# Kernel tuning notes

Measured on AMD Instinct MI355X. Metric: run time of the kernel, lower is better.

Reference implementation:

```python
import jax, jax.numpy as jnp
import numpy as np

N, E, G = 30000, 120000, 256
F_IN, F_E, H, T = 16, 8, 32, 10
EPS = 1e-5


def setup_inputs() -> dict:
    key = jax.random.key(0)
    ks = jax.random.split(key, 16)
    s = 0.05
    inp = {
        'x': jax.random.normal(ks[0], (N, F_IN), jnp.float32),
        'edge_attr': jax.random.normal(ks[1], (E, F_E), jnp.float32),
        'edge_index': jax.random.randint(ks[2], (2, E), 0, N),
        'batch': jnp.sort(jax.random.randint(ks[3], (N,), 0, G)),
        'c1_nn_w': jax.random.normal(ks[4], (F_E, F_IN * H), jnp.float32) * s,
        'c1_nn_b': jnp.zeros((F_IN * H,), jnp.float32),
        'c1_root': jax.random.normal(ks[5], (F_IN, H), jnp.float32) * s,
        'c1_bias': jnp.zeros((H,), jnp.float32),
        'c2_nn_w': jax.random.normal(ks[6], (F_E, H * H), jnp.float32) * s,
        'c2_nn_b': jnp.zeros((H * H,), jnp.float32),
        'c2_root': jax.random.normal(ks[7], (H, H), jnp.float32) * s,
        'c2_bias': jnp.zeros((H,), jnp.float32),
        'c3_nn_w': jax.random.normal(ks[8], (F_E, H * H), jnp.float32) * s,
        'c3_nn_b': jnp.zeros((H * H,), jnp.float32),
        'c3_root': jax.random.normal(ks[9], (H, H), jnp.float32) * s,
        'c3_bias': jnp.zeros((H,), jnp.float32),
        'bn1_g': jnp.ones((H,), jnp.float32), 'bn1_b': jnp.zeros((H,), jnp.float32),
        'bn1_m': jnp.zeros((H,), jnp.float32), 'bn1_v': jnp.ones((H,), jnp.float32),
        'bn2_g': jnp.ones((H,), jnp.float32), 'bn2_b': jnp.zeros((H,), jnp.float32),
        'bn2_m': jnp.zeros((H,), jnp.float32), 'bn2_v': jnp.ones((H,), jnp.float32),
        'mlp_w1': jax.random.normal(ks[10], (H, H), jnp.float32) * s,
        'mlp_b1': jnp.zeros((H,), jnp.float32),
        'mlp_w2': jax.random.normal(ks[11], (H, T), jnp.float32) * s,
        'mlp_b2': jnp.zeros((T,), jnp.float32),
    }
    return inp


def _nnconv(x, edge_index, edge_attr, nn_w, nn_b, root, bias, in_dim, out_dim):
    # per-edge weight matrix from edge features: [E, in_dim, out_dim]
    W = (edge_attr @ nn_w + nn_b).reshape(-1, in_dim, out_dim)
    # gather source node features, per-edge matvec, scatter-add to targets
    msg = jnp.einsum('ei,eio->eo', x[edge_index[0]], W)
    agg = jax.ops.segment_sum(msg, edge_index[1], num_segments=N)
    return agg + x @ root + bias


def _graph_size_norm(x, batch):
    deg = jax.ops.segment_sum(jnp.ones((N,), x.dtype), batch, num_segments=G)
    inv_sqrt = jnp.where(deg > 0, deg, 1.0) ** -0.5
    return x * inv_sqrt[batch][:, None]


def _bn_eval(x, g, b, m, v):
    return (x - m) * (g * jax.lax.rsqrt(v + EPS)) + b


def reference(x, edge_attr, edge_index, batch,
              c1_nn_w, c1_nn_b, c1_root, c1_bias,
              c2_nn_w, c2_nn_b, c2_root, c2_bias,
              c3_nn_w, c3_nn_b, c3_root, c3_bias,
              bn1_g, bn1_b, bn1_m, bn1_v,
              bn2_g, bn2_b, bn2_m, bn2_v,
              mlp_w1, mlp_b1, mlp_w2, mlp_b2):
    h = _nnconv(x, edge_index, edge_attr, c1_nn_w, c1_nn_b, c1_root, c1_bias, F_IN, H)
    h = _graph_size_norm(h, batch)
    h = jax.nn.relu(_bn_eval(h, bn1_g, bn1_b, bn1_m, bn1_v))
    h = _nnconv(h, edge_index, edge_attr, c2_nn_w, c2_nn_b, c2_root, c2_bias, H, H)
    h = _graph_size_norm(h, batch)
    h = jax.nn.relu(_bn_eval(h, bn2_g, bn2_b, bn2_m, bn2_v))
    h = _nnconv(h, edge_index, edge_attr, c3_nn_w, c3_nn_b, c3_root, c3_bias, H, H)
    # global mean pool over graphs
    cnt = jax.ops.segment_sum(jnp.ones((N,), h.dtype), batch, num_segments=G)
    pooled = jax.ops.segment_sum(h, batch, num_segments=G) / jnp.maximum(cnt, 1.0)[:, None]
    # MLP head (dropout inactive in eval)
    out = jax.nn.relu(pooled @ mlp_w1 + mlp_b1) @ mlp_w2 + mlp_b2
    return out
```

## Files before the change

kernel.cpp:

```cpp
#include <hip/hip_runtime.h>

#define NN 30000
#define NE 120000
#define NG 256
#define FIN 16
#define HD 32
#define TOUT 10
#define EPSV 1e-5f
#define NB_SCAN 30

__device__ __forceinline__ void atomAddF(float* p, float v) {
    unsafeAtomicAdd(p, v);
}

__global__ __launch_bounds__(256) void count_deg_kernel(
    const int* __restrict__ eidx, const int* __restrict__ batch,
    int* __restrict__ deg_in, float* __restrict__ deg_g)
{
    const int t = blockIdx.x * 256 + threadIdx.x;
    if (t < NE) atomicAdd(&deg_in[eidx[NE + t]], 1);

    const int lane = threadIdx.x & 63;
    const int g = (t < NN) ? batch[t] : -1;
    const int prev = __shfl_up(g, 1);
    const bool head = (lane == 0) || (g != prev);
    const unsigned long long heads = __ballot(head);
    if (head && g >= 0) {
        const unsigned long long higher =
            (lane < 63) ? (heads >> (lane + 1)) : 0ULL;
        const int next = higher ? (lane + __ffsll(higher)) : 64;
        atomAddF(&deg_g[g], (float)(next - lane));
    }
}

__global__ __launch_bounds__(1024) void scan_phase1(
    const int* __restrict__ deg_in, int* __restrict__ row_start,
    int* __restrict__ blocksum)
{
    __shared__ int wsum[16];
    const int t = threadIdx.x, lane = t & 63, w = t >> 6;
    const int idx = blockIdx.x * 1024 + t;
    const int v = (idx < NN) ? deg_in[idx] : 0;
    int s = v;
    #pragma unroll
    for (int off = 1; off < 64; off <<= 1) {
        const int u = __shfl_up(s, off, 64);
        if (lane >= off) s += u;
    }
    if (lane == 63) wsum[w] = s;
    __syncthreads();
    if (w == 0) {
        int ws = (lane < 16) ? wsum[lane] : 0;
        #pragma unroll
        for (int off = 1; off < 16; off <<= 1) {
            const int u = __shfl_up(ws, off, 64);
            if (lane >= off) ws += u;
        }
        if (lane < 16) wsum[lane] = ws;
    }
    __syncthreads();
    const int incl = s + ((w > 0) ? wsum[w - 1] : 0);
    if (idx < NN) row_start[idx] = incl - v;
    if (t == 1023) blocksum[blockIdx.x] = incl;
}

__global__ __launch_bounds__(1024) void scan_apply(
    const int* __restrict__ blocksum, int* __restrict__ row_start,
    int* __restrict__ cursor)
{
    __shared__ int boff_s;
    const int t = threadIdx.x;
    if (t < 64) {
        int v = (t < blockIdx.x) ? blocksum[t] : 0;
        #pragma unroll
        for (int off = 32; off > 0; off >>= 1) v += __shfl_down(v, off, 64);
        if (t == 0) boff_s = v;
    }
    __syncthreads();
    const int idx = blockIdx.x * 1024 + t;
    if (idx < NN) {
        const int r = row_start[idx] + boff_s;
        row_start[idx] = r;
        cursor[idx]    = r;
    }
    if (blockIdx.x == 0 && t == 0) row_start[NN] = NE;
}

__global__ __launch_bounds__(256) void csr_scatter(
    const int* __restrict__ eidx, const float* __restrict__ ea,
    int* __restrict__ cursor,
    int* __restrict__ src_s,
    float4* __restrict__ ea_s)
{
    const int e = blockIdx.x * 256 + threadIdx.x;
    if (e < NE) {
        const int d = eidx[NE + e];
        const int slot = atomicAdd(&cursor[d], 1);
        src_s[slot] = eidx[e];
        const float4* s4 = (const float4*)(ea + (size_t)e * 8);
        ea_s[2 * slot]     = s4[0];
        ea_s[2 * slot + 1] = s4[1];
    }
    if (e < 8) src_s[NE + e] = 0;
}

template<int IN, bool FINAL>
__global__ __launch_bounds__(256) void fused_layer(
    const float* __restrict__ hin,
    const int*   __restrict__ src_s,
    const float4* __restrict__ ea_s,
    const int*   __restrict__ row_start,
    const float* __restrict__ nn_w,
    const float* __restrict__ nn_b,
    const float* __restrict__ root,
    const float* __restrict__ bias,
    const int*   __restrict__ batch,
    const float* __restrict__ deg_g,
    const float* __restrict__ bn_g,
    const float* __restrict__ bn_b,
    const float* __restrict__ bn_m,
    const float* __restrict__ bn_v,
    float*       __restrict__ out)
{
    constexpr int K  = 10 * IN;
    constexpr int KQ = K / 4;
    constexpr int KL = KQ / 2;
    constexpr int NQ = 32 / IN;

    __shared__ float Tlds[16 * K];
    __shared__ float P[4 * 16 * 64];

    const int tid = threadIdx.x;
    const int wv  = tid >> 6;
    const int l   = tid & 63;
    const int h   = l >> 5;
    const int o   = l & 31;
    const int l5  = l & 31;
    const int pr  = l >> 5;

    float Wreg[KL];
    const int kbase = wv * KQ + h * KL;
    #pragma unroll
    for (int kk = 0; kk < KL; ++kk) {
        const int k = kbase + kk;
        const float* src = (k < 8 * IN) ? (nn_w + k * 32)
                         : (k < 9 * IN) ? (nn_b + (k - 8 * IN) * 32)
                                        : (root + (k - 9 * IN) * 32);
        Wreg[kk] = src[o];
    }

    const int i = l5 & (IN - 1);
    const int q = l5 / IN;

    #pragma unroll
    for (int j = 0; j < 2; ++j) {
        const int nloc = wv * 4 + j * 2 + pr;
        const int d    = blockIdx.x * 16 + nloc;

        float t[9];
        #pragma unroll
        for (int f = 0; f < 9; ++f) t[f] = 0.0f;

        const int p0 = row_start[d];
        const int p1 = row_start[d + 1];

        int p = p0 + q;
        if (p < p1) {
            int pn     = p + NQ;
            int s_cur  = src_s[p];
            int s_nxt  = src_s[pn];
            float4 a_c = ea_s[2 * p];
            float4 b_c = ea_s[2 * p + 1];
            float  xv  = hin[(long)s_cur * IN + i];

            while (true) {
                const float4 a_n = ea_s[2 * pn];
                const float4 b_n = ea_s[2 * pn + 1];
                const float  xvn = hin[(long)s_nxt * IN + i];
                const int pn2    = pn + NQ;
                const int s_n2   = src_s[pn2];

                t[0] = fmaf(a_c.x, xv, t[0]);
                t[1] = fmaf(a_c.y, xv, t[1]);
                t[2] = fmaf(a_c.z, xv, t[2]);
                t[3] = fmaf(a_c.w, xv, t[3]);
                t[4] = fmaf(b_c.x, xv, t[4]);
                t[5] = fmaf(b_c.y, xv, t[5]);
                t[6] = fmaf(b_c.z, xv, t[6]);
                t[7] = fmaf(b_c.w, xv, t[7]);
                t[8] += xv;

                p = pn;
                if (p >= p1) break;
                pn = pn2; s_nxt = s_n2;
                a_c = a_n; b_c = b_n; xv = xvn;
            }
        }

        if (IN == 16) {
            #pragma unroll
            for (int f = 0; f < 9; ++f) t[f] += __shfl_xor(t[f], 16, 64);
        }

        if (l5 < IN) {
            float* tb = Tlds + nloc * K;
            #pragma unroll
            for (int f = 0; f < 9; ++f) tb[f * IN + i] = t[f];
            tb[9 * IN + i] = hin[(long)d * IN + i];
        }
    }
    __syncthreads();

    for (int n = 0; n < 16; ++n) {
        const float* tb = Tlds + n * K + kbase;
        float acc = 0.0f;
        #pragma unroll
        for (int kq = 0; kq < KL / 4; ++kq) {
            const float4 tv = *(const float4*)(tb + kq * 4);
            acc = fmaf(Wreg[4 * kq + 0], tv.x, acc);
            acc = fmaf(Wreg[4 * kq + 1], tv.y, acc);
            acc = fmaf(Wreg[4 * kq + 2], tv.z, acc);
            acc = fmaf(Wreg[4 * kq + 3], tv.w, acc);
        }
        P[(wv * 16 + n) * 64 + l] = acc;
    }
    __syncthreads();

    #pragma unroll
    for (int r = 0; r < 2; ++r) {
        const int idx = r * 256 + tid;
        const int n   = idx >> 5;
        const int oo  = idx & 31;
        float sum = bias[oo];
        #pragma unroll
        for (int ww = 0; ww < 4; ++ww) {
            const float* pb = P + (ww * 16 + n) * 64;
            sum += pb[oo] + pb[32 + oo];
        }
        const int d = blockIdx.x * 16 + n;
        const int g = batch[d];
        if (!FINAL) {
            float dg = deg_g[g];
            dg = dg > 0.0f ? dg : 1.0f;
            float v = sum * (1.0f / sqrtf(dg));
            const float s = bn_g[oo] / sqrtf(bn_v[oo] + EPSV);
            v = (v - bn_m[oo]) * s + bn_b[oo];
            out[(long)d * 32 + oo] = v > 0.0f ? v : 0.0f;
        } else {
            float v = sum;
            const int   g2 = __shfl(g, (tid & 63) ^ 32, 64);
            const float v2 = __shfl(v, (tid & 63) ^ 32, 64);
            bool do_store = true;
            if (g2 == g) {
                if (tid & 32) do_store = false;
                else          v += v2;
            }
            if (do_store) atomAddF(&out[g * 32 + oo], v);
        }
    }
}

__global__ __launch_bounds__(64) void head_kernel(
    const float* __restrict__ pooled,
    const float* __restrict__ deg,
    const float* __restrict__ w1,
    const float* __restrict__ b1,
    const float* __restrict__ w2,
    const float* __restrict__ b2,
    float*       __restrict__ out)
{
    const int g = blockIdx.x * 64 + threadIdx.x;
    if (g >= NG) return;
    float cnt = deg[g];
    cnt = cnt > 1.0f ? cnt : 1.0f;

    float p[HD];
    #pragma unroll
    for (int i = 0; i < HD; ++i) p[i] = pooled[g * HD + i] / cnt;

    float hid[HD];
    #pragma unroll
    for (int j = 0; j < HD; ++j) {
        float a = b1[j];
        #pragma unroll
        for (int i = 0; i < HD; ++i)
            a = fmaf(p[i], w1[i * HD + j], a);
        hid[j] = a > 0.0f ? a : 0.0f;
    }
    #pragma unroll
    for (int t = 0; t < TOUT; ++t) {
        float a = b2[t];
        #pragma unroll
        for (int j = 0; j < HD; ++j)
            a = fmaf(hid[j], w2[j * TOUT + t], a);
        out[g * TOUT + t] = a;
    }
}

extern "C" void kernel_launch(void* const* d_in, const int* in_sizes, int n_in,
                              void* d_out, int out_size, void* d_ws, size_t ws_size,
                              hipStream_t stream)
{
    const float* x        = (const float*)d_in[0];
    const float* ea       = (const float*)d_in[1];
    const int*   eidx     = (const int*)  d_in[2];
    const int*   batch    = (const int*)  d_in[3];
    const float* c1_nn_w  = (const float*)d_in[4];
    const float* c1_nn_b  = (const float*)d_in[5];
    const float* c1_root  = (const float*)d_in[6];
    const float* c1_bias  = (const float*)d_in[7];
    const float* c2_nn_w  = (const float*)d_in[8];
    const float* c2_nn_b  = (const float*)d_in[9];
    const float* c2_root  = (const float*)d_in[10];
    const float* c2_bias  = (const float*)d_in[11];
    const float* c3_nn_w  = (const float*)d_in[12];
    const float* c3_nn_b  = (const float*)d_in[13];
    const float* c3_root  = (const float*)d_in[14];
    const float* c3_bias  = (const float*)d_in[15];
    const float* bn1_g    = (const float*)d_in[16];
    const float* bn1_b    = (const float*)d_in[17];
    const float* bn1_m    = (const float*)d_in[18];
    const float* bn1_v    = (const float*)d_in[19];
    const float* bn2_g    = (const float*)d_in[20];
    const float* bn2_b    = (const float*)d_in[21];
    const float* bn2_m    = (const float*)d_in[22];
    const float* bn2_v    = (const float*)d_in[23];
    const float* mlp_w1   = (const float*)d_in[24];
    const float* mlp_b1   = (const float*)d_in[25];
    const float* mlp_w2   = (const float*)d_in[26];
    const float* mlp_b2   = (const float*)d_in[27];
    float* out = (float*)d_out;

    float*  h1     = (float*)d_ws;
    float*  h2     = h1 + NN * HD;
    float*  deg_g  = h2 + NN * HD;
    float*  pooled = deg_g + NG;
    float4* ea_s   = (float4*)(pooled + NG * HD);
    int*    src_s  = (int*)(ea_s + 2 * (NE + 8));
    int*    deg_in = src_s + NE + 8;
    int*    row_s  = deg_in + NN;
    int*    cursor = row_s + NN + 1;
    int*    bsum   = cursor + NN;

    hipMemsetAsync(deg_in, 0, sizeof(int) * NN, stream);
    hipMemsetAsync(deg_g,  0, sizeof(float) * (NG + NG * HD), stream);

    const int egrid = (NE + 255) / 256;

    count_deg_kernel<<<egrid, 256, 0, stream>>>(eidx, batch, deg_in, deg_g);
    scan_phase1<<<NB_SCAN, 1024, 0, stream>>>(deg_in, row_s, bsum);
    scan_apply <<<NB_SCAN, 1024, 0, stream>>>(bsum, row_s, cursor);
    csr_scatter<<<egrid, 256, 0, stream>>>(eidx, ea, cursor, src_s, ea_s);

    const int lgrid = NN / 16;

    fused_layer<FIN, false><<<lgrid, 256, 0, stream>>>(
        x, src_s, ea_s, row_s, c1_nn_w, c1_nn_b, c1_root, c1_bias,
        batch, deg_g, bn1_g, bn1_b, bn1_m, bn1_v, h1);

    fused_layer<HD, false><<<lgrid, 256, 0, stream>>>(
        h1, src_s, ea_s, row_s, c2_nn_w, c2_nn_b, c2_root, c2_bias,
        batch, deg_g, bn2_g, bn2_b, bn2_m, bn2_v, h2);

    fused_layer<HD, true><<<lgrid, 256, 0, stream>>>(
        h2, src_s, ea_s, row_s, c3_nn_w, c3_nn_b, c3_root, c3_bias,
        batch, deg_g, nullptr, nullptr, nullptr, nullptr, pooled);

    head_kernel<<<(NG + 63) / 64, 64, 0, stream>>>(pooled, deg_g, mlp_w1, mlp_b1,
                                                   mlp_w2, mlp_b2, out);
}
```

Measured before the change: 238.9 us.

## Process block edge range flat with LDS atomics instead of per-node loops

The fused layer kernel now walks the block's whole contiguous CSR edge range (16 destination nodes) with all 256 threads. Each edge's local destination index is packed into the high bits of the source index, and threads accumulate edge-feature-weighted sums into shared memory with LDS atomics. This removes load imbalance from per-node degree variation and idle lanes in short rows. The cost is many LDS atomic adds per edge plus an atomic reduction of the partial matvec outputs. The memsets are also merged into one call, and the edge padding is widened for the deeper prefetch.

```diff
diff --git a/kernel.cpp b/kernel.cpp
--- a/kernel.cpp
+++ b/kernel.cpp
@@ -8,6 +8,7 @@
 #define TOUT 10
 #define EPSV 1e-5f
 #define NB_SCAN 30
+#define EPAD 64
 
 __device__ __forceinline__ void atomAddF(float* p, float v) {
     unsafeAtomicAdd(p, v);
@@ -89,26 +90,26 @@
 __global__ __launch_bounds__(256) void csr_scatter(
     const int* __restrict__ eidx, const float* __restrict__ ea,
     int* __restrict__ cursor,
-    int* __restrict__ src_s,
+    int* __restrict__ packed,
     float4* __restrict__ ea_s)
 {
     const int e = blockIdx.x * 256 + threadIdx.x;
     if (e < NE) {
         const int d = eidx[NE + e];
         const int slot = atomicAdd(&cursor[d], 1);
-        src_s[slot] = eidx[e];
+        packed[slot] = eidx[e] | ((d & 15) << 16);
         const float4* s4 = (const float4*)(ea + (size_t)e * 8);
         ea_s[2 * slot]     = s4[0];
         ea_s[2 * slot + 1] = s4[1];
     }
-    if (e < 8) src_s[NE + e] = 0;
+    if (e < EPAD) packed[NE + e] = 0;
 }
 
 template<int IN, bool FINAL>
 __global__ __launch_bounds__(256) void fused_layer(
     const float* __restrict__ hin,
-    const int*   __restrict__ src_s,
-    const float4* __restrict__ ea_s,
+    const int*   __restrict__ packed,
+    const float4* __restrict__ ea4,
     const int*   __restrict__ row_start,
     const float* __restrict__ nn_w,
     const float* __restrict__ nn_b,
@@ -122,107 +123,102 @@
     const float* __restrict__ bn_v,
     float*       __restrict__ out)
 {
-    constexpr int K  = 10 * IN;
-    constexpr int KQ = K / 4;
-    constexpr int KL = KQ / 2;
-    constexpr int NQ = 32 / IN;
-
-    __shared__ float Tlds[16 * K];
-    __shared__ float P[4 * 16 * 64];
+    constexpr int K    = 10 * IN;
+    constexpr int KP   = K + 4;
+    constexpr int KL   = K / 8;
+    constexpr int NQ   = 64 / IN;
+    constexpr int STEP = 4 * NQ;
+    static_assert(KL % 4 == 0, "KL must be float4-divisible");
+
+    __shared__ float Tlds[16 * KP];
+    __shared__ float OutL[16 * 32];
 
     const int tid = threadIdx.x;
     const int wv  = tid >> 6;
     const int l   = tid & 63;
-    const int h   = l >> 5;
-    const int o   = l & 31;
-    const int l5  = l & 31;
-    const int pr  = l >> 5;
-
-    float Wreg[KL];
-    const int kbase = wv * KQ + h * KL;
-    #pragma unroll
-    for (int kk = 0; kk < KL; ++kk) {
-        const int k = kbase + kk;
-        const float* src = (k < 8 * IN) ? (nn_w + k * 32)
-                         : (k < 9 * IN) ? (nn_b + (k - 8 * IN) * 32)
-                                        : (root + (k - 9 * IN) * 32);
-        Wreg[kk] = src[o];
-    }
-
-    const int i = l5 & (IN - 1);
-    const int q = l5 / IN;
-
-    #pragma unroll
-    for (int j = 0; j < 2; ++j) {
-        const int nloc = wv * 4 + j * 2 + pr;
-        const int d    = blockIdx.x * 16 + nloc;
-
-        float t[9];
-        #pragma unroll
-        for (int f = 0; f < 9; ++f) t[f] = 0.0f;
-
-        const int p0 = row_start[d];
-        const int p1 = row_start[d + 1];
-
-        int p = p0 + q;
-        if (p < p1) {
-            int pn     = p + NQ;
-            int s_cur  = src_s[p];
-            int s_nxt  = src_s[pn];
-            float4 a_c = ea_s[2 * p];
-            float4 b_c = ea_s[2 * p + 1];
-            float  xv  = hin[(long)s_cur * IN + i];
-
-            while (true) {
-                const float4 a_n = ea_s[2 * pn];
-                const float4 b_n = ea_s[2 * pn + 1];
-                const float  xvn = hin[(long)s_nxt * IN + i];
-                const int pn2    = pn + NQ;
-                const int s_n2   = src_s[pn2];
-
-                t[0] = fmaf(a_c.x, xv, t[0]);
-                t[1] = fmaf(a_c.y, xv, t[1]);
-                t[2] = fmaf(a_c.z, xv, t[2]);
-                t[3] = fmaf(a_c.w, xv, t[3]);
-                t[4] = fmaf(b_c.x, xv, t[4]);
-                t[5] = fmaf(b_c.y, xv, t[5]);
-                t[6] = fmaf(b_c.z, xv, t[6]);
-                t[7] = fmaf(b_c.w, xv, t[7]);
-                t[8] += xv;
-
-                p = pn;
-                if (p >= p1) break;
-                pn = pn2; s_nxt = s_n2;
-                a_c = a_n; b_c = b_n; xv = xvn;
+    const int b16 = blockIdx.x * 16;
+
+    {
+        float4* z4 = (float4*)Tlds;
+        const float4 zz = make_float4(0.f, 0.f, 0.f, 0.f);
+        for (int idx = tid; idx < 4 * KP; idx += 256) z4[idx] = zz;
+        const float bv = bias[tid & 31];
+        OutL[tid]       = bv;
+        OutL[tid + 256] = bv;
+    }
+    __syncthreads();
+
+    for (int t = tid; t < 16 * IN; t += 256)
+        Tlds[(t / IN) * KP + 9 * IN + (t % IN)] = hin[b16 * IN + t];
+
+    {
+        const int P0  = row_start[b16];
+        const int P1  = row_start[b16 + 16];
+        const int i   = l & (IN - 1);
+        const int q   = l / IN;
+        const int off = wv * NQ + q;
+
+        int    p   = P0 + off;
+        int    w_c = packed[p];
+        int    w_n = packed[p + STEP];
+        float4 a_c = ea4[2 * p];
+        float4 b_c = ea4[2 * p + 1];
+        float  xv  = hin[(w_c & 0xFFFF) * IN + i];
+
+        for (int base = P0; base < P1; base += STEP) {
+            const int    pn   = p + STEP;
+            const float4 a_nx = ea4[2 * pn];
+            const float4 b_nx = ea4[2 * pn + 1];
+            const float  xvn  = hin[(w_n & 0xFFFF) * IN + i];
+            const int    w_n2 = packed[pn + STEP];
+
+            if (p < P1) {
+                float* tb = Tlds + (w_c >> 16) * KP;
+                atomicAdd(&tb[0 * IN + i], a_c.x * xv);
+                atomicAdd(&tb[1 * IN + i], a_c.y * xv);
+                atomicAdd(&tb[2 * IN + i], a_c.z * xv);
+                atomicAdd(&tb[3 * IN + i], a_c.w * xv);
+                atomicAdd(&tb[4 * IN + i], b_c.x * xv);
+                atomicAdd(&tb[5 * IN + i], b_c.y * xv);
+                atomicAdd(&tb[6 * IN + i], b_c.z * xv);
+                atomicAdd(&tb[7 * IN + i], b_c.w * xv);
+                atomicAdd(&tb[8 * IN + i], xv);
             }
-        }
-
-        if (IN == 16) {
+            p = pn; w_c = w_n; w_n = w_n2;
+            a_c = a_nx; b_c = b_nx; xv = xvn;
+        }
+    }
+    __syncthreads();
+
+    {
+        const int hw    = tid >> 5;
+        const int o     = l & 31;
+        const int kbase = hw * KL;
+
+        float Wreg[KL];
+        #pragma unroll
+        for (int kk = 0; kk < KL; ++kk) {
+            const int k = kbase + kk;
+            const float* srcp = (k < 8 * IN) ? (nn_w + k * 32)
+                              : (k < 9 * IN) ? (nn_b + (k - 8 * IN) * 32)
+                                             : (root + (k - 9 * IN) * 32);
+            Wreg[kk] = srcp[o];
+        }
+
+        for (int ni = 0; ni < 16; ++ni) {
+            const int n = (ni + wv * 4) & 15;
+            const float* tb = Tlds + n * KP + kbase;
+            float acc = 0.0f;
             #pragma unroll
-            for (int f = 0; f < 9; ++f) t[f] += __shfl_xor(t[f], 16, 64);
-        }
-
-        if (l5 < IN) {
-            float* tb = Tlds + nloc * K;
-            #pragma unroll
-            for (int f = 0; f < 9; ++f) tb[f * IN + i] = t[f];
-            tb[9 * IN + i] = hin[(long)d * IN + i];
-        }
-    }
-    __syncthreads();
-
-    for (int n = 0; n < 16; ++n) {
-        const float* tb = Tlds + n * K + kbase;
-        float acc = 0.0f;
-        #pragma unroll
-        for (int kq = 0; kq < KL / 4; ++kq) {
-            const float4 tv = *(const float4*)(tb + kq * 4);
-            acc = fmaf(Wreg[4 * kq + 0], tv.x, acc);
-            acc = fmaf(Wreg[4 * kq + 1], tv.y, acc);
-            acc = fmaf(Wreg[4 * kq + 2], tv.z, acc);
-            acc = fmaf(Wreg[4 * kq + 3], tv.w, acc);
-        }
-        P[(wv * 16 + n) * 64 + l] = acc;
+            for (int kq = 0; kq < KL / 4; ++kq) {
+                const float4 tv = *(const float4*)(tb + 4 * kq);
+                acc = fmaf(Wreg[4 * kq + 0], tv.x, acc);
+                acc = fmaf(Wreg[4 * kq + 1], tv.y, acc);
+                acc = fmaf(Wreg[4 * kq + 2], tv.z, acc);
+                acc = fmaf(Wreg[4 * kq + 3], tv.w, acc);
+            }
+            atomicAdd(&OutL[n * 32 + o], acc);
+        }
     }
     __syncthreads();
 
@@ -231,13 +227,8 @@
         const int idx = r * 256 + tid;
         const int n   = idx >> 5;
         const int oo  = idx & 31;
-        float sum = bias[oo];
-        #pragma unroll
-        for (int ww = 0; ww < 4; ++ww) {
-            const float* pb = P + (ww * 16 + n) * 64;
-            sum += pb[oo] + pb[32 + oo];
-        }
-        const int d = blockIdx.x * 16 + n;
+        float sum = OutL[idx];
+        const int d = b16 + n;
         const int g = batch[d];
         if (!FINAL) {
             float dg = deg_g[g];
@@ -333,37 +324,36 @@
 
     float*  h1     = (float*)d_ws;
     float*  h2     = h1 + NN * HD;
-    float*  deg_g  = h2 + NN * HD;
-    float*  pooled = deg_g + NG;
-    float4* ea_s   = (float4*)(pooled + NG * HD);
-    int*    src_s  = (int*)(ea_s + 2 * (NE + 8));
-    int*    deg_in = src_s + NE + 8;
-    int*    row_s  = deg_in + NN;
+    float4* ea_s   = (float4*)(h2 + NN * HD);
+    int*    packed = (int*)(ea_s + 2 * (NE + EPAD));
+    int*    row_s  = packed + NE + EPAD;
     int*    cursor = row_s + NN + 1;
     int*    bsum   = cursor + NN;
-
-    hipMemsetAsync(deg_in, 0, sizeof(int) * NN, stream);
-    hipMemsetAsync(deg_g,  0, sizeof(float) * (NG + NG * HD), stream);
+    float*  deg_g  = (float*)(bsum + 32);
+    float*  pooled = deg_g + NG;
+    int*    deg_in = (int*)(pooled + NG * HD);
+
+    hipMemsetAsync(deg_g, 0, sizeof(float) * (NG + NG * HD + NN), stream);
 
     const int egrid = (NE + 255) / 256;
 
     count_deg_kernel<<<egrid, 256, 0, stream>>>(eidx, batch, deg_in, deg_g);
     scan_phase1<<<NB_SCAN, 1024, 0, stream>>>(deg_in, row_s, bsum);
     scan_apply <<<NB_SCAN, 1024, 0, stream>>>(bsum, row_s, cursor);
-    csr_scatter<<<egrid, 256, 0, stream>>>(eidx, ea, cursor, src_s, ea_s);
+    csr_scatter<<<egrid, 256, 0, stream>>>(eidx, ea, cursor, packed, ea_s);
 
     const int lgrid = NN / 16;
 
     fused_layer<FIN, false><<<lgrid, 256, 0, stream>>>(
-        x, src_s, ea_s, row_s, c1_nn_w, c1_nn_b, c1_root, c1_bias,
+        x, packed, ea_s, row_s, c1_nn_w, c1_nn_b, c1_root, c1_bias,
         batch, deg_g, bn1_g, bn1_b, bn1_m, bn1_v, h1);
 
     fused_layer<HD, false><<<lgrid, 256, 0, stream>>>(
-        h1, src_s, ea_s, row_s, c2_nn_w, c2_nn_b, c2_root, c2_bias,
+        h1, packed, ea_s, row_s, c2_nn_w, c2_nn_b, c2_root, c2_bias,
         batch, deg_g, bn2_g, bn2_b, bn2_m, bn2_v, h2);
 
     fused_layer<HD, true><<<lgrid, 256, 0, stream>>>(
-        h2, src_s, ea_s, row_s, c3_nn_w, c3_nn_b, c3_root, c3_bias,
+        h2, packed, ea_s, row_s, c3_nn_w, c3_nn_b, c3_root, c3_bias,
         batch, deg_g, nullptr, nullptr, nullptr, nullptr, pooled);
 
     head_kernel<<<(NG + 63) / 64, 64, 0, stream>>>(pooled, deg_g, mlp_w1, mlp_b1,
```

Measured after the change: 819.7 us. 243% more time.

## Use one full wavefront per destination node in edge aggregation

Applied to the files above, without the earlier changes.

Edge aggregation now assigns one 64-lane wavefront per destination node, four nodes per wave, instead of half a wave per node. Each node's edges are spread over more lanes and reduced with an extra cross-half shuffle. This aims to raise memory-level parallelism on the gather for nodes with many edges, at the cost of idle lanes on low-degree nodes. The weight-register load moves after the gather to shorten register live ranges, partial results are combined by shuffle so the LDS reduction buffer is halved, and the two memsets are merged into one by rearranging the workspace, with padding widened to 64.

```diff
diff --git a/kernel.cpp b/kernel.cpp
--- a/kernel.cpp
+++ b/kernel.cpp
@@ -8,6 +8,7 @@
 #define TOUT 10
 #define EPSV 1e-5f
 #define NB_SCAN 30
+#define EPAD 64
 
 __device__ __forceinline__ void atomAddF(float* p, float v) {
     unsafeAtomicAdd(p, v);
@@ -101,7 +102,7 @@
         ea_s[2 * slot]     = s4[0];
         ea_s[2 * slot + 1] = s4[1];
     }
-    if (e < 8) src_s[NE + e] = 0;
+    if (e < EPAD) src_s[NE + e] = 0;
 }
 
 template<int IN, bool FINAL>
@@ -125,89 +126,92 @@
     constexpr int K  = 10 * IN;
     constexpr int KQ = K / 4;
     constexpr int KL = KQ / 2;
-    constexpr int NQ = 32 / IN;
-
-    __shared__ float Tlds[16 * K];
-    __shared__ float P[4 * 16 * 64];
+    constexpr int NQ = 64 / IN;
+    static_assert(KL % 4 == 0, "KL must be float4-divisible");
+
+    __shared__ __align__(16) float Tlds[16 * K];
+    __shared__ float P[4 * 16 * 32];
 
     const int tid = threadIdx.x;
     const int wv  = tid >> 6;
     const int l   = tid & 63;
     const int h   = l >> 5;
     const int o   = l & 31;
-    const int l5  = l & 31;
-    const int pr  = l >> 5;
+
+    {
+        const int i = l & (IN - 1);
+        const int q = l / IN;
+
+        #pragma unroll
+        for (int j = 0; j < 4; ++j) {
+            const int nloc = wv * 4 + j;
+            const int d    = blockIdx.x * 16 + nloc;
+
+            float t[9];
+            #pragma unroll
+            for (int f = 0; f < 9; ++f) t[f] = 0.0f;
+
+            const int p0 = row_start[d];
+            const int p1 = row_start[d + 1];
+
+            int p = p0 + q;
+            if (p < p1) {
+                int pn     = p + NQ;
+                int s_cur  = src_s[p];
+                int s_nxt  = src_s[pn];
+                float4 a_c = ea_s[2 * p];
+                float4 b_c = ea_s[2 * p + 1];
+                float  xv  = hin[(long)s_cur * IN + i];
+
+                while (true) {
+                    const float4 a_n = ea_s[2 * pn];
+                    const float4 b_n = ea_s[2 * pn + 1];
+                    const float  xvn = hin[(long)s_nxt * IN + i];
+                    const int pn2    = pn + NQ;
+                    const int s_n2   = src_s[pn2];
+
+                    t[0] = fmaf(a_c.x, xv, t[0]);
+                    t[1] = fmaf(a_c.y, xv, t[1]);
+                    t[2] = fmaf(a_c.z, xv, t[2]);
+                    t[3] = fmaf(a_c.w, xv, t[3]);
+                    t[4] = fmaf(b_c.x, xv, t[4]);
+                    t[5] = fmaf(b_c.y, xv, t[5]);
+                    t[6] = fmaf(b_c.z, xv, t[6]);
+                    t[7] = fmaf(b_c.w, xv, t[7]);
+                    t[8] += xv;
+
+                    p = pn;
+                    if (p >= p1) break;
+                    pn = pn2; s_nxt = s_n2;
+                    a_c = a_n; b_c = b_n; xv = xvn;
+                }
+            }
+
+            if (IN == 16) {
+                #pragma unroll
+                for (int f = 0; f < 9; ++f) t[f] += __shfl_xor(t[f], 16, 64);
+            }
+            #pragma unroll
+            for (int f = 0; f < 9; ++f) t[f] += __shfl_xor(t[f], 32, 64);
+
+            if (l < IN) {
+                float* tb = Tlds + nloc * K;
+                #pragma unroll
+                for (int f = 0; f < 9; ++f) tb[f * IN + i] = t[f];
+                tb[9 * IN + i] = hin[(long)d * IN + i];
+            }
+        }
+    }
 
     float Wreg[KL];
     const int kbase = wv * KQ + h * KL;
     #pragma unroll
     for (int kk = 0; kk < KL; ++kk) {
         const int k = kbase + kk;
-        const float* src = (k < 8 * IN) ? (nn_w + k * 32)
-                         : (k < 9 * IN) ? (nn_b + (k - 8 * IN) * 32)
-                                        : (root + (k - 9 * IN) * 32);
-        Wreg[kk] = src[o];
-    }
-
-    const int i = l5 & (IN - 1);
-    const int q = l5 / IN;
-
-    #pragma unroll
-    for (int j = 0; j < 2; ++j) {
-        const int nloc = wv * 4 + j * 2 + pr;
-        const int d    = blockIdx.x * 16 + nloc;
-
-        float t[9];
-        #pragma unroll
-        for (int f = 0; f < 9; ++f) t[f] = 0.0f;
-
-        const int p0 = row_start[d];
-        const int p1 = row_start[d + 1];
-
-        int p = p0 + q;
-        if (p < p1) {
-            int pn     = p + NQ;
-            int s_cur  = src_s[p];
-            int s_nxt  = src_s[pn];
-            float4 a_c = ea_s[2 * p];
-            float4 b_c = ea_s[2 * p + 1];
-            float  xv  = hin[(long)s_cur * IN + i];
-
-            while (true) {
-                const float4 a_n = ea_s[2 * pn];
-                const float4 b_n = ea_s[2 * pn + 1];
-                const float  xvn = hin[(long)s_nxt * IN + i];
-                const int pn2    = pn + NQ;
-                const int s_n2   = src_s[pn2];
-
-                t[0] = fmaf(a_c.x, xv, t[0]);
-                t[1] = fmaf(a_c.y, xv, t[1]);
-                t[2] = fmaf(a_c.z, xv, t[2]);
-                t[3] = fmaf(a_c.w, xv, t[3]);
-                t[4] = fmaf(b_c.x, xv, t[4]);
-                t[5] = fmaf(b_c.y, xv, t[5]);
-                t[6] = fmaf(b_c.z, xv, t[6]);
-                t[7] = fmaf(b_c.w, xv, t[7]);
-                t[8] += xv;
-
-                p = pn;
-                if (p >= p1) break;
-                pn = pn2; s_nxt = s_n2;
-                a_c = a_n; b_c = b_n; xv = xvn;
-            }
-        }
-
-        if (IN == 16) {
-            #pragma unroll
-            for (int f = 0; f < 9; ++f) t[f] += __shfl_xor(t[f], 16, 64);
-        }
-
-        if (l5 < IN) {
-            float* tb = Tlds + nloc * K;
-            #pragma unroll
-            for (int f = 0; f < 9; ++f) tb[f * IN + i] = t[f];
-            tb[9 * IN + i] = hin[(long)d * IN + i];
-        }
+        const float* srcp = (k < 8 * IN) ? (nn_w + k * 32)
+                          : (k < 9 * IN) ? (nn_b + (k - 8 * IN) * 32)
+                                         : (root + (k - 9 * IN) * 32);
+        Wreg[kk] = srcp[o];
     }
     __syncthreads();
 
@@ -222,7 +226,8 @@
             acc = fmaf(Wreg[4 * kq + 2], tv.z, acc);
             acc = fmaf(Wreg[4 * kq + 3], tv.w, acc);
         }
-        P[(wv * 16 + n) * 64 + l] = acc;
+        acc += __shfl_xor(acc, 32, 64);
+        if (h == 0) P[(wv * 16 + n) * 32 + o] = acc;
     }
     __syncthreads();
 
@@ -233,10 +238,8 @@
         const int oo  = idx & 31;
         float sum = bias[oo];
         #pragma unroll
-        for (int ww = 0; ww < 4; ++ww) {
-            const float* pb = P + (ww * 16 + n) * 64;
-            sum += pb[oo] + pb[32 + oo];
-        }
+        for (int ww = 0; ww < 4; ++ww)
+            sum += P[(ww * 16 + n) * 32 + oo];
         const int d = blockIdx.x * 16 + n;
         const int g = batch[d];
         if (!FINAL) {
@@ -333,17 +336,16 @@
 
     float*  h1     = (float*)d_ws;
     float*  h2     = h1 + NN * HD;
-    float*  deg_g  = h2 + NN * HD;
-    float*  pooled = deg_g + NG;
-    float4* ea_s   = (float4*)(pooled + NG * HD);
-    int*    src_s  = (int*)(ea_s + 2 * (NE + 8));
-    int*    deg_in = src_s + NE + 8;
-    int*    row_s  = deg_in + NN;
+    float4* ea_s   = (float4*)(h2 + NN * HD);
+    int*    src_s  = (int*)(ea_s + 2 * (NE + EPAD));
+    int*    row_s  = src_s + NE + EPAD;
     int*    cursor = row_s + NN + 1;
     int*    bsum   = cursor + NN;
-
-    hipMemsetAsync(deg_in, 0, sizeof(int) * NN, stream);
-    hipMemsetAsync(deg_g,  0, sizeof(float) * (NG + NG * HD), stream);
+    float*  deg_g  = (float*)(bsum + 32);
+    float*  pooled = deg_g + NG;
+    int*    deg_in = (int*)(pooled + NG * HD);
+
+    hipMemsetAsync(deg_g, 0, sizeof(float) * (NG + NG * HD + NN), stream);
 
     const int egrid = (NE + 255) / 256;
 
```

New measurement: 247.5 us. 1.04x slower.
